# Optimization experiments

Hardware: AMD Instinct MI355X
Metric: run time of the kernel (lower is better)

The kernel has to match this reference:

```python
import jax, jax.numpy as jnp
import numpy as np

B, T, C, H = 16, 2048, 1024, 64

def setup_inputs() -> dict:
    key = jax.random.key(0)
    kx, kq, kk, kv = jax.random.split(key, 4)
    s = 0.02
    return {
        "x": jax.random.normal(kx, (B, T, C), dtype=jnp.float32),
        "Wq": jax.random.normal(kq, (C, H), dtype=jnp.float32) * s,
        "Wk": jax.random.normal(kk, (C, H), dtype=jnp.float32) * s,
        "Wv": jax.random.normal(kv, (C, H), dtype=jnp.float32) * s,
    }

def reference(x, Wq, Wk, Wv):
    Bc, Tc, Cc = x.shape
    q = x @ Wq  # [B,T,H]
    k = x @ Wk  # [B,T,H]
    v = x @ Wv  # [B,T,H]
    # NOTE: original scales by n_embed^{-0.5} (C), not head_size^{-0.5}
    wei = jnp.einsum("bth,bsh->bts", q, k) * (Cc ** -0.5)  # [B,T,T]
    causal = jnp.tril(jnp.ones((Tc, Tc), dtype=bool))
    wei = jnp.where(causal, wei, -jnp.inf)
    wei = jax.nn.softmax(wei, axis=-1)
    # dropout is identity in eval mode
    out = jnp.einsum("bts,bsh->bth", wei, v)  # [B,T,H]
    return out
```

## Files before the change

### kernel.cpp

```cpp
#include <hip/hip_runtime.h>

typedef __attribute__((ext_vector_type(8))) short short8;
typedef __attribute__((ext_vector_type(4))) float float4v;

__device__ inline short f2bf(float f) {
    union { float f; unsigned int u; } c; c.f = f;
    unsigned int u = c.u;
    unsigned int r = (u + 0x7fffu + ((u >> 16) & 1u)) >> 16;
    return (short)r;
}

__device__ inline void gl2lds16(const short* g, short* l) {
    __builtin_amdgcn_global_load_lds(
        (const __attribute__((address_space(1))) unsigned int*)g,
        (__attribute__((address_space(3))) unsigned int*)l, 16, 0, 0);
}


__global__ __launch_bounds__(256) void wconv_kernel(
    const float* __restrict__ Wq, const float* __restrict__ Wk,
    const float* __restrict__ Wv, short* __restrict__ Wt_s)
{
    __shared__ short Ls[64 * 72];
    const int w  = blockIdx.x >> 4;
    const int c  = blockIdx.x & 15;
    const int k0 = c * 64;
    const float* W = (w == 0) ? Wq : (w == 1) ? Wk : Wv;
    const int tid = threadIdx.x;

#pragma unroll
    for (int i = 0; i < 4; i++) {
        int kk = (tid >> 4) + i * 16;
        int c4 = (tid & 15) * 4;
        float4 v = *(const float4*)&W[(size_t)(k0 + kk) * 64 + c4];
        Ls[kk * 72 + c4 + 0] = f2bf(v.x);
        Ls[kk * 72 + c4 + 1] = f2bf(v.y);
        Ls[kk * 72 + c4 + 2] = f2bf(v.z);
        Ls[kk * 72 + c4 + 3] = f2bf(v.w);
    }
    __syncthreads();
    const int n  = tid >> 2;
    const int k8 = (tid & 3) * 16;
    short8 o0, o1;
#pragma unroll
    for (int j = 0; j < 8; j++) o0[j] = Ls[(k8 + j) * 72 + n];
#pragma unroll
    for (int j = 0; j < 8; j++) o1[j] = Ls[(k8 + 8 + j) * 72 + n];
    const int gn = w * 64 + n;
    short* base = &Wt_s[((size_t)c * 192 + gn) * 64];
    int g0 = k8 >> 3;
    *(short8*)&base[((g0    ) ^ (gn & 7)) * 8] = o0;
    *(short8*)&base[((g0 + 1) ^ (gn & 7)) * 8] = o1;
}

__global__ __launch_bounds__(256) void qkv_kernel(
    const float* __restrict__ x, const short* __restrict__ Wt_s,
    short* __restrict__ qo, short* __restrict__ k_s, short* __restrict__ vT_t)
{
    __shared__ short As[2][64 * 72];
    __shared__ short Bs[2][192 * 64];

    const int tid  = threadIdx.x;
    const int wave = tid >> 6, lane = tid & 63;
    const int quad = lane >> 4, l16 = lane & 15;
    const int m0   = blockIdx.x * 64;

    float4v acc[4][3];
#pragma unroll
    for (int mf = 0; mf < 4; mf++)
#pragma unroll
        for (int nt = 0; nt < 3; nt++) acc[mf][nt] = (float4v)0.0f;

    const int arow = tid >> 2;
    const int acol = (tid & 3) * 16;
    const float* ap = &x[(size_t)(m0 + arow) * 1024 + acol];
    const int lofs = lane * 8;

    {
        float4 x0 = *(const float4*)(ap + 0);
        float4 x1 = *(const float4*)(ap + 4);
        float4 x2 = *(const float4*)(ap + 8);
        float4 x3 = *(const float4*)(ap + 12);
        const short* gsrc = Wt_s + ((size_t)wave * 48) * 64;
        short* ldst = &Bs[0][wave * 48 * 64];
#pragma unroll
        for (int i = 0; i < 6; i++)
            gl2lds16(gsrc + i * 512 + lofs, ldst + i * 512 + lofs);
        short8 av0, av1;
        av0[0]=f2bf(x0.x); av0[1]=f2bf(x0.y); av0[2]=f2bf(x0.z); av0[3]=f2bf(x0.w);
        av0[4]=f2bf(x1.x); av0[5]=f2bf(x1.y); av0[6]=f2bf(x1.z); av0[7]=f2bf(x1.w);
        av1[0]=f2bf(x2.x); av1[1]=f2bf(x2.y); av1[2]=f2bf(x2.z); av1[3]=f2bf(x2.w);
        av1[4]=f2bf(x3.x); av1[5]=f2bf(x3.y); av1[6]=f2bf(x3.z); av1[7]=f2bf(x3.w);
        *(short8*)&As[0][arow * 72 + acol]     = av0;
        *(short8*)&As[0][arow * 72 + acol + 8] = av1;
    }
    __syncthreads();

    int cur = 0;
    for (int kc = 0; kc < 1024; kc += 64) {
        const int nxt = cur ^ 1;
        const bool pf = (kc + 64) < 1024;
        float4 x0, x1, x2, x3;
        if (pf) {
            x0 = *(const float4*)(ap + kc + 64);
            x1 = *(const float4*)(ap + kc + 68);
            x2 = *(const float4*)(ap + kc + 72);
            x3 = *(const float4*)(ap + kc + 76);
            const short* gsrc = Wt_s + ((size_t)((kc >> 6) + 1) * 192 + wave * 48) * 64;
            short* ldst = &Bs[nxt][wave * 48 * 64];
#pragma unroll
            for (int i = 0; i < 6; i++)
                gl2lds16(gsrc + i * 512 + lofs, ldst + i * 512 + lofs);
        }
        const short* Asc = As[cur];
        const short* Bsc = Bs[cur];
#pragma unroll
        for (int kc2 = 0; kc2 < 2; kc2++) {
            short8 a0 = *(const short8*)&Asc[(     l16) * 72 + kc2*32 + quad*8];
            short8 a1 = *(const short8*)&Asc[(16 + l16) * 72 + kc2*32 + quad*8];
            short8 a2 = *(const short8*)&Asc[(32 + l16) * 72 + kc2*32 + quad*8];
            short8 a3 = *(const short8*)&Asc[(48 + l16) * 72 + kc2*32 + quad*8];
#pragma unroll
            for (int nt = 0; nt < 3; nt++) {
                int brow = wave * 48 + nt * 16 + l16;
                int g = kc2 * 4 + quad;
                short8 bf = *(const short8*)&Bsc[brow * 64 + (g ^ (brow & 7)) * 8];
                acc[0][nt] = __builtin_amdgcn_mfma_f32_16x16x32_bf16(a0, bf, acc[0][nt], 0, 0, 0);
                acc[1][nt] = __builtin_amdgcn_mfma_f32_16x16x32_bf16(a1, bf, acc[1][nt], 0, 0, 0);
                acc[2][nt] = __builtin_amdgcn_mfma_f32_16x16x32_bf16(a2, bf, acc[2][nt], 0, 0, 0);
                acc[3][nt] = __builtin_amdgcn_mfma_f32_16x16x32_bf16(a3, bf, acc[3][nt], 0, 0, 0);
            }
        }
        if (pf) {
            short8 av0, av1;
            av0[0]=f2bf(x0.x); av0[1]=f2bf(x0.y); av0[2]=f2bf(x0.z); av0[3]=f2bf(x0.w);
            av0[4]=f2bf(x1.x); av0[5]=f2bf(x1.y); av0[6]=f2bf(x1.z); av0[7]=f2bf(x1.w);
            av1[0]=f2bf(x2.x); av1[1]=f2bf(x2.y); av1[2]=f2bf(x2.z); av1[3]=f2bf(x2.w);
            av1[4]=f2bf(x3.x); av1[5]=f2bf(x3.y); av1[6]=f2bf(x3.z); av1[7]=f2bf(x3.w);
            *(short8*)&As[nxt][arow * 72 + acol]     = av0;
            *(short8*)&As[nxt][arow * 72 + acol + 8] = av1;
        }
        __syncthreads();
        cur = nxt;
    }
#pragma unroll
    for (int mf = 0; mf < 4; mf++) {
#pragma unroll
        for (int nt = 0; nt < 3; nt++) {
            int g = wave * 48 + nt * 16 + l16;
#pragma unroll
            for (int r = 0; r < 4; r++) {
                int row = m0 + mf * 16 + quad * 4 + r;
                short val = f2bf(acc[mf][nt][r]);
                if (g < 64) {
                    qo[(size_t)row * 64 + g] = val;
                } else if (g < 128) {
                    int h = g - 64;
                    k_s[(size_t)row * 64 + (((h >> 3) ^ (row & 7)) * 8 + (h & 7))] = val;
                } else {
                    int h = g - 128;
                    int bb = row >> 11, tt = row & 2047;
                    int tc = tt >> 6, tl = tt & 63;
                    vT_t[(((size_t)bb * 32 + tc) * 64 + h) * 64 +
                         (((tl >> 3) ^ (h & 7)) * 8 + (tl & 7))] = val;
                }
            }
        }
    }
}

#define SCALE_LOG2E 0.04508422132f

__global__ __launch_bounds__(256) void attn_kernel(
    const short* __restrict__ q, const short* __restrict__ k_s,
    const short* __restrict__ vT_t, float* __restrict__ out)
{
    __shared__ short Ks[2][64 * 64];
    __shared__ short Vs[2][64 * 64];
    __shared__ short Ps[64 * 72];

    const int tid  = threadIdx.x;
    const int wave = tid >> 6, lane = tid & 63;
    const int quad = lane >> 4, l16 = lane & 15;

    int b, qt;
    if (blockIdx.x < 256) { b = blockIdx.x >> 4; qt = 16 + (blockIdx.x & 15); }
    else { int t2 = blockIdx.x - 256; b = t2 >> 4; qt = 15 - (t2 & 15); }

    const short* kb = k_s  + (size_t)b * 2048 * 64;
    const short* vb = vT_t + (size_t)b * 32 * 64 * 64;

    const short* qrow = q + ((size_t)b * 2048 + qt*64 + wave*16 + l16) * 64;
    short8 qf0 = *(const short8*)&qrow[quad*8];
    short8 qf1 = *(const short8*)&qrow[32 + quad*8];

    float4v oacc[4];
#pragma unroll
    for (int t = 0; t < 4; t++) oacc[t] = (float4v)0.0f;
    float l_i[4] = {0.f, 0.f, 0.f, 0.f};

    const int tg   = qt*64 + wave*16 + quad*4;
    const int jmax = qt;
    const int lofs = lane * 8;

    {
        const short* kg = kb + ((size_t)wave * 16) * 64;
        short* kl = &Ks[0][wave * 16 * 64];
        gl2lds16(kg +       lofs, kl +       lofs);
        gl2lds16(kg + 512 + lofs, kl + 512 + lofs);
        const short* vg = vb + ((size_t)wave * 16) * 64;
        short* vl = &Vs[0][wave * 16 * 64];
        gl2lds16(vg +       lofs, vl +       lofs);
        gl2lds16(vg + 512 + lofs, vl + 512 + lofs);
    }
    __syncthreads();

    int cur = 0;
    for (int j = 0; j <= jmax; j++) {
        const int nxt = cur ^ 1;
        if (j < jmax) {
            const short* kg = kb + ((size_t)(j + 1) * 64 + wave * 16) * 64;
            short* kl = &Ks[nxt][wave * 16 * 64];
            gl2lds16(kg +       lofs, kl +       lofs);
            gl2lds16(kg + 512 + lofs, kl + 512 + lofs);
            const short* vg = vb + ((size_t)(j + 1) * 64 + wave * 16) * 64;
            short* vl = &Vs[nxt][wave * 16 * 64];
            gl2lds16(vg +       lofs, vl +       lofs);
            gl2lds16(vg + 512 + lofs, vl + 512 + lofs);
        }
        const short* Ksc = Ks[cur];
        const short* Vsc = Vs[cur];

        float4v sacc[4];
#pragma unroll
        for (int t = 0; t < 4; t++) sacc[t] = (float4v)0.0f;
#pragma unroll
        for (int t = 0; t < 4; t++) {
            int brow = t*16 + l16;
            short8 b0 = *(const short8*)&Ksc[brow * 64 + ((    quad) ^ (brow & 7)) * 8];
            short8 b1 = *(const short8*)&Ksc[brow * 64 + ((4 + quad) ^ (brow & 7)) * 8];
            sacc[t] = __builtin_amdgcn_mfma_f32_16x16x32_bf16(qf0, b0, sacc[t], 0, 0, 0);
            sacc[t] = __builtin_amdgcn_mfma_f32_16x16x32_bf16(qf1, b1, sacc[t], 0, 0, 0);
        }
        if (j == jmax) {
#pragma unroll
            for (int t = 0; t < 4; t++) {
                int sg = j*64 + t*16 + l16;
#pragma unroll
                for (int r = 0; r < 4; r++) {
                    float p = exp2f(sacc[t][r] * SCALE_LOG2E);
                    if (sg > tg + r) p = 0.0f;
                    sacc[t][r] = p;
                    l_i[r] += p;
                }
            }
        } else {
#pragma unroll
            for (int t = 0; t < 4; t++)
#pragma unroll
                for (int r = 0; r < 4; r++) {
                    float p = exp2f(sacc[t][r] * SCALE_LOG2E);
                    sacc[t][r] = p;
                    l_i[r] += p;
                }
        }
#pragma unroll
        for (int t = 0; t < 4; t++)
#pragma unroll
            for (int r = 0; r < 4; r++)
                Ps[(wave*16 + quad*4 + r) * 72 + t*16 + l16] = f2bf(sacc[t][r]);
#pragma unroll
        for (int kc = 0; kc < 2; kc++) {
            short8 af = *(const short8*)&Ps[(wave*16 + l16) * 72 + kc*32 + quad*8];
#pragma unroll
            for (int t = 0; t < 4; t++) {
                int drow = t*16 + l16;
                short8 bf = *(const short8*)&Vsc[drow * 64 + ((kc*4 + quad) ^ (drow & 7)) * 8];
                oacc[t] = __builtin_amdgcn_mfma_f32_16x16x32_bf16(af, bf, oacc[t], 0, 0, 0);
            }
        }
        __syncthreads();
        cur = nxt;
    }
#pragma unroll
    for (int off = 1; off < 16; off <<= 1)
#pragma unroll
        for (int r = 0; r < 4; r++)
            l_i[r] += __shfl_xor(l_i[r], off, 64);
#pragma unroll
    for (int r = 0; r < 4; r++) {
        float inv = 1.0f / l_i[r];
        int row = qt*64 + wave*16 + quad*4 + r;
#pragma unroll
        for (int t = 0; t < 4; t++)
            out[((size_t)b * 2048 + row) * 64 + t*16 + l16] = oacc[t][r] * inv;
    }
}

extern "C" void kernel_launch(void* const* d_in, const int* in_sizes, int n_in,
                              void* d_out, int out_size, void* d_ws, size_t ws_size,
                              hipStream_t stream)
{
    const float* x  = (const float*)d_in[0];
    const float* Wq = (const float*)d_in[1];
    const float* Wk = (const float*)d_in[2];
    const float* Wv = (const float*)d_in[3];

    short* qw   = (short*)d_ws;
    short* ks   = qw + (size_t)32768 * 64;
    short* vTt  = ks + (size_t)32768 * 64;
    short* Wts  = vTt + (size_t)32768 * 64;
    float* out  = (float*)d_out;

    hipLaunchKernelGGL(wconv_kernel, dim3(48), dim3(256), 0, stream,
                       Wq, Wk, Wv, Wts);
    hipLaunchKernelGGL(qkv_kernel, dim3(512), dim3(256), 0, stream,
                       x, Wts, qw, ks, vTt);
    hipLaunchKernelGGL(attn_kernel, dim3(512), dim3(256), 0, stream,
                       qw, ks, vTt, out);
}
```

Baseline: 251.5 us.

## Drop LDS staging in QKV projection; load MFMA fragments directly from global

The QKV projection kernel no longer stages x and the transposed weights through double-buffered shared memory with barriers. Each wave now computes a 32x96 output tile and loads its MFMA operand fragments straight from global memory, with a register prefetch of the next x chunk. The weight conversion kernel writes a plain row-major [192][1024] bf16 layout instead of the swizzled chunked layout. This removes LDS traffic and __syncthreads, but weights are re-read from global/L2 by every wave, and the access pattern becomes strided.

```diff
diff --git a/kernel.cpp b/kernel.cpp
--- a/kernel.cpp
+++ b/kernel.cpp
@@ -10,6 +10,13 @@
     return (short)r;
 }
 
+__device__ inline short8 pack8(float4 a, float4 b) {
+    short8 r;
+    r[0]=f2bf(a.x); r[1]=f2bf(a.y); r[2]=f2bf(a.z); r[3]=f2bf(a.w);
+    r[4]=f2bf(b.x); r[5]=f2bf(b.y); r[6]=f2bf(b.z); r[7]=f2bf(b.w);
+    return r;
+}
+
 __device__ inline void gl2lds16(const short* g, short* l) {
     __builtin_amdgcn_global_load_lds(
         (const __attribute__((address_space(1))) unsigned int*)g,
@@ -19,7 +26,7 @@
 
 __global__ __launch_bounds__(256) void wconv_kernel(
     const float* __restrict__ Wq, const float* __restrict__ Wk,
-    const float* __restrict__ Wv, short* __restrict__ Wt_s)
+    const float* __restrict__ Wv, short* __restrict__ Wt)
 {
     __shared__ short Ls[64 * 72];
     const int w  = blockIdx.x >> 4;
@@ -47,107 +54,75 @@
 #pragma unroll
     for (int j = 0; j < 8; j++) o1[j] = Ls[(k8 + 8 + j) * 72 + n];
     const int gn = w * 64 + n;
-    short* base = &Wt_s[((size_t)c * 192 + gn) * 64];
-    int g0 = k8 >> 3;
-    *(short8*)&base[((g0    ) ^ (gn & 7)) * 8] = o0;
-    *(short8*)&base[((g0 + 1) ^ (gn & 7)) * 8] = o1;
+    short* base = &Wt[(size_t)gn * 1024 + k0 + k8];
+    *(short8*)&base[0] = o0;
+    *(short8*)&base[8] = o1;
 }
 
 __global__ __launch_bounds__(256) void qkv_kernel(
-    const float* __restrict__ x, const short* __restrict__ Wt_s,
+    const float* __restrict__ x, const short* __restrict__ Wt,
     short* __restrict__ qo, short* __restrict__ k_s, short* __restrict__ vT_t)
 {
-    __shared__ short As[2][64 * 72];
-    __shared__ short Bs[2][192 * 64];
-
     const int tid  = threadIdx.x;
     const int wave = tid >> 6, lane = tid & 63;
     const int quad = lane >> 4, l16 = lane & 15;
-    const int m0   = blockIdx.x * 64;
-
-    float4v acc[4][3];
-#pragma unroll
-    for (int mf = 0; mf < 4; mf++)
-#pragma unroll
-        for (int nt = 0; nt < 3; nt++) acc[mf][nt] = (float4v)0.0f;
-
-    const int arow = tid >> 2;
-    const int acol = (tid & 3) * 16;
-    const float* ap = &x[(size_t)(m0 + arow) * 1024 + acol];
-    const int lofs = lane * 8;
-
-    {
-        float4 x0 = *(const float4*)(ap + 0);
-        float4 x1 = *(const float4*)(ap + 4);
-        float4 x2 = *(const float4*)(ap + 8);
-        float4 x3 = *(const float4*)(ap + 12);
-        const short* gsrc = Wt_s + ((size_t)wave * 48) * 64;
-        short* ldst = &Bs[0][wave * 48 * 64];
-#pragma unroll
-        for (int i = 0; i < 6; i++)
-            gl2lds16(gsrc + i * 512 + lofs, ldst + i * 512 + lofs);
-        short8 av0, av1;
-        av0[0]=f2bf(x0.x); av0[1]=f2bf(x0.y); av0[2]=f2bf(x0.z); av0[3]=f2bf(x0.w);
-        av0[4]=f2bf(x1.x); av0[5]=f2bf(x1.y); av0[6]=f2bf(x1.z); av0[7]=f2bf(x1.w);
-        av1[0]=f2bf(x2.x); av1[1]=f2bf(x2.y); av1[2]=f2bf(x2.z); av1[3]=f2bf(x2.w);
-        av1[4]=f2bf(x3.x); av1[5]=f2bf(x3.y); av1[6]=f2bf(x3.z); av1[7]=f2bf(x3.w);
-        *(short8*)&As[0][arow * 72 + acol]     = av0;
-        *(short8*)&As[0][arow * 72 + acol + 8] = av1;
-    }
-    __syncthreads();
-
-    int cur = 0;
-    for (int kc = 0; kc < 1024; kc += 64) {
-        const int nxt = cur ^ 1;
-        const bool pf = (kc + 64) < 1024;
-        float4 x0, x1, x2, x3;
-        if (pf) {
-            x0 = *(const float4*)(ap + kc + 64);
-            x1 = *(const float4*)(ap + kc + 68);
-            x2 = *(const float4*)(ap + kc + 72);
-            x3 = *(const float4*)(ap + kc + 76);
-            const short* gsrc = Wt_s + ((size_t)((kc >> 6) + 1) * 192 + wave * 48) * 64;
-            short* ldst = &Bs[nxt][wave * 48 * 64];
-#pragma unroll
-            for (int i = 0; i < 6; i++)
-                gl2lds16(gsrc + i * 512 + lofs, ldst + i * 512 + lofs);
-        }
-        const short* Asc = As[cur];
-        const short* Bsc = Bs[cur];
-#pragma unroll
-        for (int kc2 = 0; kc2 < 2; kc2++) {
-            short8 a0 = *(const short8*)&Asc[(     l16) * 72 + kc2*32 + quad*8];
-            short8 a1 = *(const short8*)&Asc[(16 + l16) * 72 + kc2*32 + quad*8];
-            short8 a2 = *(const short8*)&Asc[(32 + l16) * 72 + kc2*32 + quad*8];
-            short8 a3 = *(const short8*)&Asc[(48 + l16) * 72 + kc2*32 + quad*8];
-#pragma unroll
-            for (int nt = 0; nt < 3; nt++) {
-                int brow = wave * 48 + nt * 16 + l16;
-                int g = kc2 * 4 + quad;
-                short8 bf = *(const short8*)&Bsc[brow * 64 + (g ^ (brow & 7)) * 8];
-                acc[0][nt] = __builtin_amdgcn_mfma_f32_16x16x32_bf16(a0, bf, acc[0][nt], 0, 0, 0);
-                acc[1][nt] = __builtin_amdgcn_mfma_f32_16x16x32_bf16(a1, bf, acc[1][nt], 0, 0, 0);
-                acc[2][nt] = __builtin_amdgcn_mfma_f32_16x16x32_bf16(a2, bf, acc[2][nt], 0, 0, 0);
-                acc[3][nt] = __builtin_amdgcn_mfma_f32_16x16x32_bf16(a3, bf, acc[3][nt], 0, 0, 0);
-            }
-        }
-        if (pf) {
-            short8 av0, av1;
-            av0[0]=f2bf(x0.x); av0[1]=f2bf(x0.y); av0[2]=f2bf(x0.z); av0[3]=f2bf(x0.w);
-            av0[4]=f2bf(x1.x); av0[5]=f2bf(x1.y); av0[6]=f2bf(x1.z); av0[7]=f2bf(x1.w);
-            av1[0]=f2bf(x2.x); av1[1]=f2bf(x2.y); av1[2]=f2bf(x2.z); av1[3]=f2bf(x2.w);
-            av1[4]=f2bf(x3.x); av1[5]=f2bf(x3.y); av1[6]=f2bf(x3.z); av1[7]=f2bf(x3.w);
-            *(short8*)&As[nxt][arow * 72 + acol]     = av0;
-            *(short8*)&As[nxt][arow * 72 + acol + 8] = av1;
-        }
-        __syncthreads();
-        cur = nxt;
-    }
-#pragma unroll
-    for (int mf = 0; mf < 4; mf++) {
-#pragma unroll
-        for (int nt = 0; nt < 3; nt++) {
-            int g = wave * 48 + nt * 16 + l16;
+    const int msub = wave >> 1;
+    const int nh   = wave & 1;
+    const int m0   = blockIdx.x * 64 + msub * 32;
+    const int nc0  = nh * 96;
+
+    const float* xr0 = &x[(size_t)(m0 + l16) * 1024 + quad * 8];
+    const float* xr1 = xr0 + 16 * 1024;
+    const short* wp  = &Wt[(size_t)(nc0 + l16) * 1024 + quad * 8];
+
+    float4v acc[2][6];
+#pragma unroll
+    for (int mf = 0; mf < 2; mf++)
+#pragma unroll
+        for (int nt = 0; nt < 6; nt++) acc[mf][nt] = (float4v)0.0f;
+
+    float4 n0 = *(const float4*)(xr0);
+    float4 n1 = *(const float4*)(xr0 + 4);
+    float4 n2 = *(const float4*)(xr0 + 32);
+    float4 n3 = *(const float4*)(xr0 + 36);
+    float4 n4 = *(const float4*)(xr1);
+    float4 n5 = *(const float4*)(xr1 + 4);
+    float4 n6 = *(const float4*)(xr1 + 32);
+    float4 n7 = *(const float4*)(xr1 + 36);
+
+    for (int s = 0; s < 16; s++) {
+        short8 af00 = pack8(n0, n1);
+        short8 af01 = pack8(n2, n3);
+        short8 af10 = pack8(n4, n5);
+        short8 af11 = pack8(n6, n7);
+        if (s < 15) {
+            const float* p0 = xr0 + (size_t)(s + 1) * 64;
+            const float* p1 = xr1 + (size_t)(s + 1) * 64;
+            n0 = *(const float4*)(p0);      n1 = *(const float4*)(p0 + 4);
+            n2 = *(const float4*)(p0 + 32); n3 = *(const float4*)(p0 + 36);
+            n4 = *(const float4*)(p1);      n5 = *(const float4*)(p1 + 4);
+            n6 = *(const float4*)(p1 + 32); n7 = *(const float4*)(p1 + 36);
+        }
+        const short* wk = wp + s * 64;
+#pragma unroll
+        for (int nt = 0; nt < 6; nt++) {
+            short8 bf = *(const short8*)(wk + (size_t)nt * 16 * 1024);
+            acc[0][nt] = __builtin_amdgcn_mfma_f32_16x16x32_bf16(af00, bf, acc[0][nt], 0, 0, 0);
+            acc[1][nt] = __builtin_amdgcn_mfma_f32_16x16x32_bf16(af10, bf, acc[1][nt], 0, 0, 0);
+        }
+#pragma unroll
+        for (int nt = 0; nt < 6; nt++) {
+            short8 bf = *(const short8*)(wk + 32 + (size_t)nt * 16 * 1024);
+            acc[0][nt] = __builtin_amdgcn_mfma_f32_16x16x32_bf16(af01, bf, acc[0][nt], 0, 0, 0);
+            acc[1][nt] = __builtin_amdgcn_mfma_f32_16x16x32_bf16(af11, bf, acc[1][nt], 0, 0, 0);
+        }
+    }
+
+#pragma unroll
+    for (int mf = 0; mf < 2; mf++) {
+#pragma unroll
+        for (int nt = 0; nt < 6; nt++) {
+            int g = nc0 + nt * 16 + l16;
 #pragma unroll
             for (int r = 0; r < 4; r++) {
                 int row = m0 + mf * 16 + quad * 4 + r;
```

After: 282.1 us. +12.2%, slower.
